# Kernel optimization log

Measured on AMD Instinct MI355X. Metric: run time of the kernel, lower is better.

## Reference

```python
import jax, jax.numpy as jnp
import numpy as np

BN_EPS = 1e-5
STRIDE = 4
K_NEAREST = 16


def _fps(xyz, m):
    """Farthest point sampling. xyz: [n,3] -> indices [m] (seeded at point 0)."""
    n = xyz.shape[0]

    def body(i, state):
        dist, idxs, last = state
        d = jnp.sum((xyz - xyz[last]) ** 2, axis=-1)
        dist = jnp.minimum(dist, d)
        nxt = jnp.argmax(dist).astype(jnp.int32)
        return dist, idxs.at[i].set(nxt), nxt

    init = (jnp.full((n,), 1e10, xyz.dtype), jnp.zeros((m,), jnp.int32), jnp.int32(0))
    _, idxs, _ = jax.lax.fori_loop(1, m, body, init)
    return idxs


def _knn(q, x, k):
    """q: [m,3] queries, x: [n,3] points -> [m,k] nearest-neighbor indices."""
    d = jnp.sum((q[:, None, :] - x[None, :, :]) ** 2, axis=-1)  # [m,n]
    _, idx = jax.lax.top_k(-d, k)
    return idx


def setup_inputs() -> dict:
    key = jax.random.key(0)
    k0, k1, k2 = jax.random.split(key, 3)
    B, N, IN_CH, OUT_CH = 4, 8192, 64, 128
    events = jax.random.uniform(k0, (B, N, 4), dtype=jnp.float32)  # xyz in [0,1) + time
    features = jax.random.normal(k1, (B, N, IN_CH), dtype=jnp.float32)
    W = jax.random.normal(k2, (4 + IN_CH, OUT_CH), dtype=jnp.float32) / np.float32(np.sqrt(4 + IN_CH))
    b = jnp.zeros((OUT_CH,), jnp.float32)
    gamma = jnp.ones((OUT_CH,), jnp.float32)
    beta = jnp.zeros((OUT_CH,), jnp.float32)
    return dict(events=events, features=features, W=W, b=b, gamma=gamma, beta=beta)


def reference(events, features, W, b, gamma, beta):
    B, N, _ = events.shape
    m = N // STRIDE  # down_offsets = offsets // stride with equal-size samples
    xyz = events[..., :3]
    xyz_c = jax.lax.stop_gradient(xyz)  # indices are non-differentiable

    # farthest point sampling per cloud -> [B, m]
    down_idx = jax.vmap(lambda p: _fps(p, m))(xyz_c)
    down_xyz = jnp.take_along_axis(xyz_c, down_idx[..., None], axis=1)  # [B,m,3]
    # k nearest neighbors of each sampled point -> [B, m, K]
    idx = jax.vmap(lambda q, x: _knn(q, x, K_NEAREST))(down_xyz, xyz_c)

    down_events = jnp.take_along_axis(events, down_idx[..., None], axis=1)  # [B,m,4]
    grouped_events = jax.vmap(lambda e, i: e[i])(events, idx)               # [B,m,K,4]
    grouped_events_norm = grouped_events - down_events[:, :, None, :]
    grouped_features = jax.vmap(lambda f, i: f[i])(features, idx)           # [B,m,K,in_ch]
    g = jnp.concatenate([grouped_events_norm, grouped_features], axis=-1)   # [B,m,K,4+in_ch]

    # Linear -> BatchNorm1d (training batch stats over all points & neighbors) -> ReLU
    h = jnp.einsum('bmkc,cd->bmkd', g, W) + b
    mu = jnp.mean(h, axis=(0, 1, 2))
    var = jnp.var(h, axis=(0, 1, 2))
    h = (h - mu) * jax.lax.rsqrt(var + BN_EPS) * gamma + beta
    h = jax.nn.relu(h)

    down_features = jnp.max(h, axis=2)  # max-pool over K neighbors -> [B,m,out_ch]
    return down_events, down_features
```

## Files before the change

### kernel.cpp

```cpp
#include <hip/hip_runtime.h>

#define N_PTS 8192
#define M_PTS 2048
#define K_NN 16
#define IN_CH 64
#define G_CH 68
#define OUT_CH 128
#define KCAP 128

__device__ __forceinline__ float subrn(float a, float b) {
    float r; asm("v_sub_f32 %0, %1, %2" : "=v"(r) : "v"(a), "v"(b)); return r;
}
__device__ __forceinline__ float mulrn(float a, float b) {
    float r; asm("v_mul_f32 %0, %1, %2" : "=v"(r) : "v"(a), "v"(b)); return r;
}
__device__ __forceinline__ float addrn(float a, float b) {
    float r; asm("v_add_f32 %0, %1, %2" : "=v"(r) : "v"(a), "v"(b)); return r;
}
__device__ __forceinline__ float sqdist_rn(float ax, float ay, float az,
                                           float bx, float by, float bz) {
    float dx = subrn(ax, bx);
    float dy = subrn(ay, by);
    float dz = subrn(az, bz);
    return addrn(addrn(mulrn(dx, dx), mulrn(dy, dy)), mulrn(dz, dz));
}

typedef float v2f __attribute__((ext_vector_type(2)));
__device__ __forceinline__ v2f pk_add(v2f a, v2f b) {
    v2f r; asm("v_pk_add_f32 %0, %1, %2" : "=v"(r) : "v"(a), "v"(b)); return r;
}
__device__ __forceinline__ v2f pk_mul(v2f a, v2f b) {
    v2f r; asm("v_pk_mul_f32 %0, %1, %2" : "=v"(r) : "v"(a), "v"(b)); return r;
}

template <int CTRL>
__device__ __forceinline__ float movdpp_f(float x) {
    int r = __builtin_amdgcn_mov_dpp(__float_as_int(x), CTRL, 0xf, 0xf, true);
    return __int_as_float(r);
}
template <int CTRL, int RM>
__device__ __forceinline__ float dppmaxf_m(float x) {
    int r = __builtin_amdgcn_update_dpp(0, __float_as_int(x), CTRL, RM, 0xf, false);
    return fmaxf(x, __int_as_float(r));
}
__device__ __forceinline__ float wave_max64(float x) {
    x = fmaxf(x, movdpp_f<0xB1>(x));
    x = fmaxf(x, movdpp_f<0x4E>(x));
    x = fmaxf(x, movdpp_f<0x141>(x));
    x = fmaxf(x, movdpp_f<0x140>(x));
    x = dppmaxf_m<0x142, 0xa>(x);
    x = dppmaxf_m<0x143, 0xc>(x);
    return x;
}
__device__ __forceinline__ float group8_max(float x) {
    x = fmaxf(x, movdpp_f<0xB1>(x));
    x = fmaxf(x, movdpp_f<0x4E>(x));
    x = fmaxf(x, movdpp_f<0x141>(x));
    return x;
}

__global__ __launch_bounds__(512, 2) void fps_kernel(const float4* __restrict__ events4,
                                                     int* __restrict__ down_idx,
                                                     float4* __restrict__ out_de) {
    extern __shared__ char smem[];
    float*  rv   = (float*)smem;
    int*    wsl  = (int*)(smem + 32);
    int*    ssel = (int*)(smem + 64);
    float4* spt  = (float4*)(smem + 64 + 4 * M_PTS);

    const int b = blockIdx.x;
    const int tid = threadIdx.x;
    const int wave = tid >> 6;
    const int lane = tid & 63;
    const float4* ev = events4 + (size_t)b * N_PTS;

    for (int i = tid; i < N_PTS; i += 512) spt[i] = ev[i];
    if (tid == 0) { ssel[0] = 0; wsl[0] = 0x7fffffff; wsl[1] = 0x7fffffff; }
    __syncthreads();

    v2f px[8], py[8], pz[8];
    float dist[16];
#pragma unroll
    for (int pp = 0; pp < 8; ++pp) {
        float4 f0 = spt[(2 * pp) * 512 + tid];
        float4 f1 = spt[(2 * pp + 1) * 512 + tid];
        px[pp] = (v2f){f0.x, f1.x};
        py[pp] = (v2f){f0.y, f1.y};
        pz[pp] = (v2f){f0.z, f1.z};
        dist[2 * pp] = 1e10f; dist[2 * pp + 1] = 1e10f;
    }

    int last = 0;
    for (int i = 1; i < M_PTS; ++i) {
        float4 L = spt[last];
        const float nlx = -L.x, nly = -L.y, nlz = -L.z;
        const v2f nx2 = (v2f){nlx, nlx};
        const v2f ny2 = (v2f){nly, nly};
        const v2f nz2 = (v2f){nlz, nlz};
#pragma unroll
        for (int pp = 0; pp < 8; ++pp) {
            v2f dx = pk_add(px[pp], nx2);
            v2f dy = pk_add(py[pp], ny2);
            v2f dz = pk_add(pz[pp], nz2);
            v2f s  = pk_add(pk_add(pk_mul(dx, dx), pk_mul(dy, dy)), pk_mul(dz, dz));
            dist[2 * pp]     = fminf(dist[2 * pp],     s.x);
            dist[2 * pp + 1] = fminf(dist[2 * pp + 1], s.y);
        }
        float t0[8];
#pragma unroll
        for (int j = 0; j < 8; ++j) t0[j] = fmaxf(dist[2 * j], dist[2 * j + 1]);
#pragma unroll
        for (int j = 0; j < 4; ++j) t0[j] = fmaxf(t0[2 * j], t0[2 * j + 1]);
        float bd = fmaxf(fmaxf(t0[0], t0[1]), fmaxf(t0[2], t0[3]));

        float wm = wave_max64(bd);
        if (lane == 63) rv[wave] = wm;
        __syncthreads();
        float bm = group8_max(rv[lane & 7]);

        if (bd == bm) {
            int jm = 0;
#pragma unroll
            for (int j = 15; j >= 0; --j) if (dist[j] == bd) jm = j;
            atomicMin(&wsl[i & 1], jm * 512 + tid);
        }
        __syncthreads();
        last = wsl[i & 1];
        if (tid == 0) { ssel[i] = last; wsl[(i + 1) & 1] = 0x7fffffff; }
    }
    __syncthreads();

    for (int i = tid; i < M_PTS; i += 512) {
        int s = ssel[i];
        down_idx[b * M_PTS + i] = s;
        out_de[(size_t)b * M_PTS + i] = spt[s];
    }
}

__global__ __launch_bounds__(256, 1) void knn_kernel(const float4* __restrict__ events4,
                                                     const int* __restrict__ down_idx,
                                                     int* __restrict__ knn_idx) {
    extern __shared__ char smem[];
    float2* sxy  = (float2*)smem;
    float*  sz   = (float*)(smem + N_PTS * 8);
    float*  cd   = sz + N_PTS;
    int*    ci   = (int*)(cd + 32 * KCAP);
    int*    scnt = (int*)(ci + 32 * KCAP);

    const int b    = blockIdx.x >> 6;
    const int qg   = blockIdx.x & 63;
    const int tid  = threadIdx.x;
    const int ql   = tid >> 3;
    const int part = tid & 7;

    const float4* ev = events4 + (size_t)b * N_PTS;
    for (int i = tid; i < N_PTS; i += 256) {
        float4 e = ev[i];
        sxy[i] = (float2){e.x, e.y}; sz[i] = e.z;
    }
    if (tid < 32) scnt[tid] = 0;
    __syncthreads();

    const int q  = qg * 32 + ql;
    const int qi = down_idx[b * M_PTS + q];
    const float2 qxy = sxy[qi];
    const float qx = qxy.x, qy = qxy.y, qz = sz[qi];

    const float4* sxy4 = (const float4*)sxy;
    const float2* sz2  = (const float2*)sz;

    float m1 = 1e30f, m2 = 1e30f;
    for (int i = 0; i < N_PTS / 16; ++i) {
        const int ph = i * 8 + part;
        float4 xy = sxy4[ph];
        float2 zz = sz2[ph];
        float d0 = sqdist_rn(xy.x, xy.y, zz.x, qx, qy, qz);
        float d1 = sqdist_rn(xy.z, xy.w, zz.y, qx, qy, qz);
        float lo0 = fminf(m1, d0);
        m2 = fminf(m2, fmaxf(m1, d0));
        m1 = lo0;
        float lo1 = fminf(m1, d1);
        m2 = fminf(m2, fmaxf(m1, d1));
        m1 = lo1;
    }
    const float T = group8_max(m2);

    for (int i = 0; i < N_PTS / 16; ++i) {
        const int ph = i * 8 + part;
        float4 xy = sxy4[ph];
        float2 zz = sz2[ph];
        float d0 = sqdist_rn(xy.x, xy.y, zz.x, qx, qy, qz);
        float d1 = sqdist_rn(xy.z, xy.w, zz.y, qx, qy, qz);
        if (d0 <= T) {
            int pos = atomicAdd(&scnt[ql], 1);
            if (pos < KCAP) { cd[ql * KCAP + pos] = d0; ci[ql * KCAP + pos] = 2 * ph; }
        }
        if (d1 <= T) {
            int pos = atomicAdd(&scnt[ql], 1);
            if (pos < KCAP) { cd[ql * KCAP + pos] = d1; ci[ql * KCAP + pos] = 2 * ph + 1; }
        }
    }
    __syncthreads();

    if (part == 0) {
        float nd[16]; int ni[16];
#pragma unroll
        for (int j = 0; j < 16; ++j) { nd[j] = 1e30f; ni[j] = 0x7fffffff; }
        float wmax = 1e30f; int widx = 0x7fffffff; int wslot = 0;
        const int n = scnt[ql];
        const int lim = (n <= KCAP) ? n : 0;
        for (int t = 0; t < lim; ++t) {
            float d = cd[ql * KCAP + t];
            int   p = ci[ql * KCAP + t];
            if (d < wmax || (d == wmax && p < widx)) {
#pragma unroll
                for (int j = 0; j < 16; ++j) if (j == wslot) { nd[j] = d; ni[j] = p; }
                float m_ = -1.0f; int mix_ = -1; int ms_ = 0;
#pragma unroll
                for (int j = 0; j < 16; ++j)
                    if (nd[j] > m_ || (nd[j] == m_ && ni[j] > mix_)) { m_ = nd[j]; mix_ = ni[j]; ms_ = j; }
                wmax = m_; widx = mix_; wslot = ms_;
            }
        }
        if (n > KCAP) {
            for (int p = 0; p < N_PTS; ++p) {
                float2 pxy = sxy[p];
                float d = sqdist_rn(pxy.x, pxy.y, sz[p], qx, qy, qz);
                if (d < wmax || (d == wmax && p < widx)) {
#pragma unroll
                    for (int j = 0; j < 16; ++j) if (j == wslot) { nd[j] = d; ni[j] = p; }
                    float m_ = -1.0f; int mix_ = -1; int ms_ = 0;
#pragma unroll
                    for (int j = 0; j < 16; ++j)
                        if (nd[j] > m_ || (nd[j] == m_ && ni[j] > mix_)) { m_ = nd[j]; mix_ = ni[j]; ms_ = j; }
                    wmax = m_; widx = mix_; wslot = ms_;
                }
            }
        }
        int* out = knn_idx + ((size_t)(b * M_PTS + q)) * K_NN;
#pragma unroll
        for (int j = 0; j < 16; ++j) out[j] = ni[j];
    }
}

__global__ __launch_bounds__(256, 2) void gmm_kernel(const float4* __restrict__ events4,
                                                     const float4* __restrict__ feat4,
                                                     const float* __restrict__ W,
                                                     const float* __restrict__ bias,
                                                     const int* __restrict__ knn_idx,
                                                     const float4* __restrict__ de4,
                                                     float* __restrict__ hmax_g,
                                                     float* __restrict__ hmin_g,
                                                     float* __restrict__ gsum,
                                                     float* __restrict__ gsq) {
    __shared__ __align__(16) float4 sg4[2 * 16 * 17];
    __shared__ float scomb[2 * OUT_CH];

    const int b   = blockIdx.x >> 7;
    const int qg  = blockIdx.x & 127;
    const int tid = threadIdx.x;
    const int d   = tid & 127;
    const int qs  = tid >> 7;

    float w[G_CH];
#pragma unroll
    for (int c = 0; c < G_CH; ++c) w[c] = W[c * OUT_CH + d];
    const float breg = bias[d];

    float ssum = 0.f, ssq = 0.f;

    for (int r = 0; r < 8; ++r) {
        const int base = b * M_PTS + qg * 16 + 2 * r;
        for (int j4 = tid; j4 < 2 * 16 * 17; j4 += 256) {
            int qq = j4 / 272;
            int rem = j4 - qq * 272;
            int k = rem / 17;
            int c4 = rem - k * 17;
            int nb = knn_idx[(base + qq) * K_NN + k];
            float4 v;
            if (c4 == 0) {
                float4 e = events4[(size_t)b * N_PTS + nb];
                float4 d0 = de4[base + qq];
                v = (float4){e.x - d0.x, e.y - d0.y, e.z - d0.z, e.w - d0.w};
            } else {
                v = feat4[((size_t)(b * N_PTS + nb)) * 16 + (c4 - 1)];
            }
            sg4[j4] = v;
        }
        __syncthreads();

        float hmax = -1e30f, hmin = 1e30f;
#pragma unroll
        for (int k = 0; k < 16; ++k) {
            float acc = breg;
#pragma unroll
            for (int c4 = 0; c4 < 17; ++c4) {
                float4 g = sg4[qs * 272 + k * 17 + c4];
                acc = fmaf(g.x, w[4 * c4 + 0], acc);
                acc = fmaf(g.y, w[4 * c4 + 1], acc);
                acc = fmaf(g.z, w[4 * c4 + 2], acc);
                acc = fmaf(g.w, w[4 * c4 + 3], acc);
            }
            hmax = fmaxf(hmax, acc);
            hmin = fminf(hmin, acc);
            ssum += acc;
            ssq = fmaf(acc, acc, ssq);
        }
        const size_t o = (size_t)(base + qs) * OUT_CH + d;
        hmax_g[o] = hmax;
        hmin_g[o] = hmin;
        __syncthreads();
    }

    if (qs == 1) { scomb[d] = ssum; scomb[OUT_CH + d] = ssq; }
    __syncthreads();
    if (qs == 0) {
        atomicAdd(&gsum[d], ssum + scomb[d]);
        atomicAdd(&gsq[d],  ssq  + scomb[OUT_CH + d]);
    }
}

__global__ __launch_bounds__(256) void fin_kernel(const float* __restrict__ hmax_g,
                                                  const float* __restrict__ hmin_g,
                                                  const float* __restrict__ gsum,
                                                  const float* __restrict__ gsq,
                                                  const float* __restrict__ gamma,
                                                  const float* __restrict__ beta,
                                                  float* __restrict__ out) {
    const size_t e = (size_t)blockIdx.x * 256 + threadIdx.x;
    const int d = (int)(e & 127);
    const float inv_cnt = 1.0f / 131072.0f;
    float mu  = gsum[d] * inv_cnt;
    float var = gsq[d] * inv_cnt - mu * mu;
    float a   = gamma[d] * rsqrtf(var + 1e-5f);
    float sh  = fmaf(-mu, a, beta[d]);
    float hv  = (a >= 0.f) ? hmax_g[e] : hmin_g[e];
    float r   = fmaf(a, hv, sh);
    out[32768 + e] = r > 0.f ? r : 0.f;
}

extern "C" void kernel_launch(void* const* d_in, const int* in_sizes, int n_in,
                              void* d_out, int out_size, void* d_ws, size_t ws_size,
                              hipStream_t stream) {
    const float* events   = (const float*)d_in[0];
    const float* features = (const float*)d_in[1];
    const float* W        = (const float*)d_in[2];
    const float* bias     = (const float*)d_in[3];
    const float* gamma    = (const float*)d_in[4];
    const float* beta     = (const float*)d_in[5];
    float* out = (float*)d_out;
    char* ws = (char*)d_ws;

    int*   down_idx = (int*)ws;
    int*   knn_idx  = (int*)(ws + 32768);
    float* gsum     = (float*)(ws + 32768 + 524288);
    float* gsq      = gsum + OUT_CH;
    float* hmaxg    = (float*)(ws + 558080);
    float* hming    = hmaxg + (size_t)4 * M_PTS * OUT_CH;

    (void)hipMemsetAsync(gsum, 0, 2 * OUT_CH * sizeof(float), stream);

    const size_t fps_lds = 64 + 4 * M_PTS + (size_t)N_PTS * sizeof(float4);
    fps_kernel<<<4, 512, fps_lds, stream>>>((const float4*)events, down_idx, (float4*)out);

    const size_t knn_lds = (size_t)N_PTS * 8 + (size_t)N_PTS * 4
                         + (size_t)32 * KCAP * 8 + 128;
    knn_kernel<<<256, 256, knn_lds, stream>>>((const float4*)events, down_idx, knn_idx);

    gmm_kernel<<<512, 256, 0, stream>>>((const float4*)events, (const float4*)features,
                                        W, bias, knn_idx, (const float4*)out,
                                        hmaxg, hming, gsum, gsq);

    fin_kernel<<<4096, 256, 0, stream>>>(hmaxg, hming, gsum, gsq, gamma, beta, out);
}
```

Before: 2.376 ms.

## Fuse FPS, KNN and grouped MLP into one persistent kernel with progress flags

Merges the three kernels into one launch. Four blocks run farthest point sampling and publish progress through global atomic counters. The remaining 252 blocks wait on those counters and then run KNN and the grouped linear/stat accumulation for chunks of 16 queries. This overlaps the serial FPS with the KNN and matmul work, which previously ran only after FPS finished, and drops the knn_idx round trip through global memory. KNN now uses 32 lanes per query with a single-min threshold and a larger candidate cap. The spin-waits depend on the FPS blocks being co-resident, and the looser threshold may send more queries to the slow fallback path.

```diff
diff --git a/kernel.cpp b/kernel.cpp
--- a/kernel.cpp
+++ b/kernel.cpp
@@ -6,7 +6,10 @@
 #define IN_CH 64
 #define G_CH 68
 #define OUT_CH 128
-#define KCAP 128
+#define KC 192
+#define NWK 63
+#define CHQ 16
+#define NCHUNK (M_PTS / CHQ)
 
 __device__ __forceinline__ float subrn(float a, float b) {
     float r; asm("v_sub_f32 %0, %1, %2" : "=v"(r) : "v"(a), "v"(b)); return r;
@@ -58,177 +61,201 @@
     x = fmaxf(x, movdpp_f<0x141>(x));
     return x;
 }
-
-__global__ __launch_bounds__(512, 2) void fps_kernel(const float4* __restrict__ events4,
-                                                     int* __restrict__ down_idx,
-                                                     float4* __restrict__ out_de) {
+__device__ __forceinline__ float group32_max(float x) {
+    x = fmaxf(x, movdpp_f<0xB1>(x));
+    x = fmaxf(x, movdpp_f<0x4E>(x));
+    x = fmaxf(x, movdpp_f<0x141>(x));
+    x = fmaxf(x, movdpp_f<0x140>(x));
+    x = fmaxf(x, __shfl_xor(x, 16));
+    return x;
+}
+
+__global__ __launch_bounds__(512, 2) void fused_kernel(
+        const float4* __restrict__ events4,
+        const float4* __restrict__ feat4,
+        const float*  __restrict__ W,
+        const float*  __restrict__ bias,
+        int*   __restrict__ down_idx,
+        int*   __restrict__ prog,
+        float4* __restrict__ out_de,
+        float* __restrict__ hmax_g,
+        float* __restrict__ hmin_g,
+        float* __restrict__ gsum,
+        float* __restrict__ gsq) {
     extern __shared__ char smem[];
-    float*  rv   = (float*)smem;
-    int*    wsl  = (int*)(smem + 32);
-    int*    ssel = (int*)(smem + 64);
-    float4* spt  = (float4*)(smem + 64 + 4 * M_PTS);
-
-    const int b = blockIdx.x;
     const int tid = threadIdx.x;
-    const int wave = tid >> 6;
-    const int lane = tid & 63;
+
+    if (blockIdx.x < 4) {
+        float*  rv   = (float*)smem;
+        int*    wsl  = (int*)(smem + 32);
+        int*    ssel = (int*)(smem + 64);
+        float4* spt  = (float4*)(smem + 64 + 4 * M_PTS);
+
+        const int b = blockIdx.x;
+        const int wave = tid >> 6;
+        const int lane = tid & 63;
+        const float4* ev = events4 + (size_t)b * N_PTS;
+
+        for (int i = tid; i < N_PTS; i += 512) spt[i] = ev[i];
+        if (tid == 0) {
+            ssel[0] = 0; wsl[0] = 0x7fffffff; wsl[1] = 0x7fffffff;
+            down_idx[b * M_PTS] = 0;
+        }
+        __syncthreads();
+
+        v2f px[8], py[8], pz[8];
+        float dist[16];
+#pragma unroll
+        for (int pp = 0; pp < 8; ++pp) {
+            float4 f0 = spt[(2 * pp) * 512 + tid];
+            float4 f1 = spt[(2 * pp + 1) * 512 + tid];
+            px[pp] = (v2f){f0.x, f1.x};
+            py[pp] = (v2f){f0.y, f1.y};
+            pz[pp] = (v2f){f0.z, f1.z};
+            dist[2 * pp] = 1e10f; dist[2 * pp + 1] = 1e10f;
+        }
+
+        int last = 0;
+        for (int i = 1; i < M_PTS; ++i) {
+            float4 L = spt[last];
+            const float nlx = -L.x, nly = -L.y, nlz = -L.z;
+            const v2f nx2 = (v2f){nlx, nlx};
+            const v2f ny2 = (v2f){nly, nly};
+            const v2f nz2 = (v2f){nlz, nlz};
+#pragma unroll
+            for (int pp = 0; pp < 8; ++pp) {
+                v2f dx = pk_add(px[pp], nx2);
+                v2f dy = pk_add(py[pp], ny2);
+                v2f dz = pk_add(pz[pp], nz2);
+                v2f s  = pk_add(pk_add(pk_mul(dx, dx), pk_mul(dy, dy)), pk_mul(dz, dz));
+                dist[2 * pp]     = fminf(dist[2 * pp],     s.x);
+                dist[2 * pp + 1] = fminf(dist[2 * pp + 1], s.y);
+            }
+            float t0[8];
+#pragma unroll
+            for (int j = 0; j < 8; ++j) t0[j] = fmaxf(dist[2 * j], dist[2 * j + 1]);
+#pragma unroll
+            for (int j = 0; j < 4; ++j) t0[j] = fmaxf(t0[2 * j], t0[2 * j + 1]);
+            float bd = fmaxf(fmaxf(t0[0], t0[1]), fmaxf(t0[2], t0[3]));
+
+            float wm = wave_max64(bd);
+            if (lane == 63) rv[wave] = wm;
+            __syncthreads();
+            float bm = group8_max(rv[lane & 7]);
+
+            if (bd == bm) {
+                int jm = 0;
+#pragma unroll
+                for (int j = 15; j >= 0; --j) if (dist[j] == bd) jm = j;
+                atomicMin(&wsl[i & 1], jm * 512 + tid);
+            }
+            __syncthreads();
+            last = wsl[i & 1];
+            if (tid == 0) {
+                ssel[i] = last;
+                down_idx[b * M_PTS + i] = last;
+                wsl[(i + 1) & 1] = 0x7fffffff;
+                if ((i & 31) == 31)
+                    __hip_atomic_store(prog + b, i + 1, __ATOMIC_RELEASE,
+                                       __HIP_MEMORY_SCOPE_AGENT);
+            }
+        }
+        __syncthreads();
+
+        for (int i = tid; i < M_PTS; i += 512) {
+            out_de[(size_t)b * M_PTS + i] = spt[ssel[i]];
+        }
+        return;
+    }
+
+    float2* sxy  = (float2*)smem;
+    float*  szl  = (float*)(smem + 65536);
+    float*  cd   = (float*)(smem + 98304);
+    int*    ci   = (int*)(smem + 98304 + 16 * KC * 4);
+    int*    scnt = (int*)(smem + 98304 + 32 * KC * 4);
+    int*    sqi  = (int*)(smem + 98304 + 32 * KC * 4 + 64);
+    int*    sk   = (int*)(smem + 98304 + 32 * KC * 4 + 128);
+    float4* sg4  = (float4*)(smem + 98304 + 32 * KC * 4 + 1152);
+
+    const int wk = blockIdx.x - 4;
+    const int b  = wk / NWK;
+    const int w  = wk - b * NWK;
+    const int ql   = tid >> 5;
+    const int part = tid & 31;
+    const int d  = tid & 127;
+    const int qs = tid >> 7;
+
     const float4* ev = events4 + (size_t)b * N_PTS;
-
-    for (int i = tid; i < N_PTS; i += 512) spt[i] = ev[i];
-    if (tid == 0) { ssel[0] = 0; wsl[0] = 0x7fffffff; wsl[1] = 0x7fffffff; }
-    __syncthreads();
-
-    v2f px[8], py[8], pz[8];
-    float dist[16];
-#pragma unroll
-    for (int pp = 0; pp < 8; ++pp) {
-        float4 f0 = spt[(2 * pp) * 512 + tid];
-        float4 f1 = spt[(2 * pp + 1) * 512 + tid];
-        px[pp] = (v2f){f0.x, f1.x};
-        py[pp] = (v2f){f0.y, f1.y};
-        pz[pp] = (v2f){f0.z, f1.z};
-        dist[2 * pp] = 1e10f; dist[2 * pp + 1] = 1e10f;
+    for (int i = tid; i < N_PTS; i += 512) {
+        float4 e = ev[i];
+        sxy[i] = (float2){e.x, e.y}; szl[i] = e.z;
     }
 
-    int last = 0;
-    for (int i = 1; i < M_PTS; ++i) {
-        float4 L = spt[last];
-        const float nlx = -L.x, nly = -L.y, nlz = -L.z;
-        const v2f nx2 = (v2f){nlx, nlx};
-        const v2f ny2 = (v2f){nly, nly};
-        const v2f nz2 = (v2f){nlz, nlz};
-#pragma unroll
-        for (int pp = 0; pp < 8; ++pp) {
-            v2f dx = pk_add(px[pp], nx2);
-            v2f dy = pk_add(py[pp], ny2);
-            v2f dz = pk_add(pz[pp], nz2);
-            v2f s  = pk_add(pk_add(pk_mul(dx, dx), pk_mul(dy, dy)), pk_mul(dz, dz));
-            dist[2 * pp]     = fminf(dist[2 * pp],     s.x);
-            dist[2 * pp + 1] = fminf(dist[2 * pp + 1], s.y);
-        }
-        float t0[8];
-#pragma unroll
-        for (int j = 0; j < 8; ++j) t0[j] = fmaxf(dist[2 * j], dist[2 * j + 1]);
-#pragma unroll
-        for (int j = 0; j < 4; ++j) t0[j] = fmaxf(t0[2 * j], t0[2 * j + 1]);
-        float bd = fmaxf(fmaxf(t0[0], t0[1]), fmaxf(t0[2], t0[3]));
-
-        float wm = wave_max64(bd);
-        if (lane == 63) rv[wave] = wm;
-        __syncthreads();
-        float bm = group8_max(rv[lane & 7]);
-
-        if (bd == bm) {
-            int jm = 0;
-#pragma unroll
-            for (int j = 15; j >= 0; --j) if (dist[j] == bd) jm = j;
-            atomicMin(&wsl[i & 1], jm * 512 + tid);
-        }
-        __syncthreads();
-        last = wsl[i & 1];
-        if (tid == 0) { ssel[i] = last; wsl[(i + 1) & 1] = 0x7fffffff; }
-    }
-    __syncthreads();
-
-    for (int i = tid; i < M_PTS; i += 512) {
-        int s = ssel[i];
-        down_idx[b * M_PTS + i] = s;
-        out_de[(size_t)b * M_PTS + i] = spt[s];
-    }
-}
-
-__global__ __launch_bounds__(256, 1) void knn_kernel(const float4* __restrict__ events4,
-                                                     const int* __restrict__ down_idx,
-                                                     int* __restrict__ knn_idx) {
-    extern __shared__ char smem[];
-    float2* sxy  = (float2*)smem;
-    float*  sz   = (float*)(smem + N_PTS * 8);
-    float*  cd   = sz + N_PTS;
-    int*    ci   = (int*)(cd + 32 * KCAP);
-    int*    scnt = (int*)(ci + 32 * KCAP);
-
-    const int b    = blockIdx.x >> 6;
-    const int qg   = blockIdx.x & 63;
-    const int tid  = threadIdx.x;
-    const int ql   = tid >> 3;
-    const int part = tid & 7;
-
-    const float4* ev = events4 + (size_t)b * N_PTS;
-    for (int i = tid; i < N_PTS; i += 256) {
-        float4 e = ev[i];
-        sxy[i] = (float2){e.x, e.y}; sz[i] = e.z;
-    }
-    if (tid < 32) scnt[tid] = 0;
-    __syncthreads();
-
-    const int q  = qg * 32 + ql;
-    const int qi = down_idx[b * M_PTS + q];
-    const float2 qxy = sxy[qi];
-    const float qx = qxy.x, qy = qxy.y, qz = sz[qi];
+    float wreg[G_CH];
+#pragma unroll
+    for (int c = 0; c < G_CH; ++c) wreg[c] = W[c * OUT_CH + d];
+    const float breg = bias[d];
+    float ssum = 0.f, ssq = 0.f;
 
     const float4* sxy4 = (const float4*)sxy;
-    const float2* sz2  = (const float2*)sz;
-
-    float m1 = 1e30f, m2 = 1e30f;
-    for (int i = 0; i < N_PTS / 16; ++i) {
-        const int ph = i * 8 + part;
-        float4 xy = sxy4[ph];
-        float2 zz = sz2[ph];
-        float d0 = sqdist_rn(xy.x, xy.y, zz.x, qx, qy, qz);
-        float d1 = sqdist_rn(xy.z, xy.w, zz.y, qx, qy, qz);
-        float lo0 = fminf(m1, d0);
-        m2 = fminf(m2, fmaxf(m1, d0));
-        m1 = lo0;
-        float lo1 = fminf(m1, d1);
-        m2 = fminf(m2, fmaxf(m1, d1));
-        m1 = lo1;
-    }
-    const float T = group8_max(m2);
-
-    for (int i = 0; i < N_PTS / 16; ++i) {
-        const int ph = i * 8 + part;
-        float4 xy = sxy4[ph];
-        float2 zz = sz2[ph];
-        float d0 = sqdist_rn(xy.x, xy.y, zz.x, qx, qy, qz);
-        float d1 = sqdist_rn(xy.z, xy.w, zz.y, qx, qy, qz);
-        if (d0 <= T) {
-            int pos = atomicAdd(&scnt[ql], 1);
-            if (pos < KCAP) { cd[ql * KCAP + pos] = d0; ci[ql * KCAP + pos] = 2 * ph; }
-        }
-        if (d1 <= T) {
-            int pos = atomicAdd(&scnt[ql], 1);
-            if (pos < KCAP) { cd[ql * KCAP + pos] = d1; ci[ql * KCAP + pos] = 2 * ph + 1; }
-        }
-    }
-    __syncthreads();
-
-    if (part == 0) {
-        float nd[16]; int ni[16];
-#pragma unroll
-        for (int j = 0; j < 16; ++j) { nd[j] = 1e30f; ni[j] = 0x7fffffff; }
-        float wmax = 1e30f; int widx = 0x7fffffff; int wslot = 0;
-        const int n = scnt[ql];
-        const int lim = (n <= KCAP) ? n : 0;
-        for (int t = 0; t < lim; ++t) {
-            float d = cd[ql * KCAP + t];
-            int   p = ci[ql * KCAP + t];
-            if (d < wmax || (d == wmax && p < widx)) {
-#pragma unroll
-                for (int j = 0; j < 16; ++j) if (j == wslot) { nd[j] = d; ni[j] = p; }
-                float m_ = -1.0f; int mix_ = -1; int ms_ = 0;
-#pragma unroll
-                for (int j = 0; j < 16; ++j)
-                    if (nd[j] > m_ || (nd[j] == m_ && ni[j] > mix_)) { m_ = nd[j]; mix_ = ni[j]; ms_ = j; }
-                wmax = m_; widx = mix_; wslot = ms_;
-            }
-        }
-        if (n > KCAP) {
-            for (int p = 0; p < N_PTS; ++p) {
-                float2 pxy = sxy[p];
-                float d = sqdist_rn(pxy.x, pxy.y, sz[p], qx, qy, qz);
-                if (d < wmax || (d == wmax && p < widx)) {
-#pragma unroll
-                    for (int j = 0; j < 16; ++j) if (j == wslot) { nd[j] = d; ni[j] = p; }
+    const float2* sz2  = (const float2*)szl;
+
+    for (int s = 0; s < 3; ++s) {
+        const int c = w + s * NWK;
+        if (c >= NCHUNK) break;
+        const int need = (c + 1) * CHQ;
+        while (__hip_atomic_load(prog + b, __ATOMIC_ACQUIRE,
+                                 __HIP_MEMORY_SCOPE_AGENT) < need)
+            __builtin_amdgcn_s_sleep(16);
+        if (tid < CHQ) scnt[tid] = 0;
+        __syncthreads();
+
+        const int q  = c * CHQ + ql;
+        const int qi = down_idx[b * M_PTS + q];
+        const float2 qxy = sxy[qi];
+        const float qx = qxy.x, qy = qxy.y, qz = szl[qi];
+
+        float m1 = 1e30f;
+        for (int i = 0; i < 128; ++i) {
+            const int ph = i * 32 + part;
+            float4 xy = sxy4[ph];
+            float2 zz = sz2[ph];
+            float d0 = sqdist_rn(xy.x, xy.y, zz.x, qx, qy, qz);
+            float d1 = sqdist_rn(xy.z, xy.w, zz.y, qx, qy, qz);
+            m1 = fminf(m1, fminf(d0, d1));
+        }
+        const float T = group32_max(m1);
+
+        for (int i = 0; i < 128; ++i) {
+            const int ph = i * 32 + part;
+            float4 xy = sxy4[ph];
+            float2 zz = sz2[ph];
+            float d0 = sqdist_rn(xy.x, xy.y, zz.x, qx, qy, qz);
+            float d1 = sqdist_rn(xy.z, xy.w, zz.y, qx, qy, qz);
+            if (d0 <= T) {
+                int pos = atomicAdd(&scnt[ql], 1);
+                if (pos < KC) { cd[ql * KC + pos] = d0; ci[ql * KC + pos] = 2 * ph; }
+            }
+            if (d1 <= T) {
+                int pos = atomicAdd(&scnt[ql], 1);
+                if (pos < KC) { cd[ql * KC + pos] = d1; ci[ql * KC + pos] = 2 * ph + 1; }
+            }
+        }
+        __syncthreads();
+
+        if (part == 0) {
+            float nd[16]; int ni[16];
+#pragma unroll
+            for (int j = 0; j < 16; ++j) { nd[j] = 1e30f; ni[j] = 0x7fffffff; }
+            float wmax = 1e30f; int widx = 0x7fffffff; int wslot = 0;
+            const int n = scnt[ql];
+            const int lim = (n <= KC) ? n : 0;
+            for (int t = 0; t < lim; ++t) {
+                float dv = cd[ql * KC + t];
+                int   p  = ci[ql * KC + t];
+                if (dv < wmax || (dv == wmax && p < widx)) {
+#pragma unroll
+                    for (int j = 0; j < 16; ++j) if (j == wslot) { nd[j] = dv; ni[j] = p; }
                     float m_ = -1.0f; int mix_ = -1; int ms_ = 0;
 #pragma unroll
                     for (int j = 0; j < 16; ++j)
@@ -236,88 +263,80 @@
                     wmax = m_; widx = mix_; wslot = ms_;
                 }
             }
-        }
-        int* out = knn_idx + ((size_t)(b * M_PTS + q)) * K_NN;
-#pragma unroll
-        for (int j = 0; j < 16; ++j) out[j] = ni[j];
+            if (n > KC) {
+                for (int p = 0; p < N_PTS; ++p) {
+                    float2 pxy = sxy[p];
+                    float dv = sqdist_rn(pxy.x, pxy.y, szl[p], qx, qy, qz);
+                    if (dv < wmax || (dv == wmax && p < widx)) {
+#pragma unroll
+                        for (int j = 0; j < 16; ++j) if (j == wslot) { nd[j] = dv; ni[j] = p; }
+                        float m_ = -1.0f; int mix_ = -1; int ms_ = 0;
+#pragma unroll
+                        for (int j = 0; j < 16; ++j)
+                            if (nd[j] > m_ || (nd[j] == m_ && ni[j] > mix_)) { m_ = nd[j]; mix_ = ni[j]; ms_ = j; }
+                        wmax = m_; widx = mix_; wslot = ms_;
+                    }
+                }
+            }
+            sqi[ql] = qi;
+#pragma unroll
+            for (int j = 0; j < 16; ++j) sk[ql * 16 + j] = ni[j];
+        }
+        __syncthreads();
+
+        for (int r4 = 0; r4 < 4; ++r4) {
+            for (int j4 = tid; j4 < 4 * 16 * 17; j4 += 512) {
+                int qq  = j4 / 272;
+                int rem = j4 - qq * 272;
+                int k   = rem / 17;
+                int c4  = rem - k * 17;
+                int qlo = r4 * 4 + qq;
+                int nb  = sk[qlo * 16 + k];
+                float4 v;
+                if (c4 == 0) {
+                    float4 e  = events4[(size_t)b * N_PTS + nb];
+                    float4 d0 = events4[(size_t)b * N_PTS + sqi[qlo]];
+                    v = (float4){e.x - d0.x, e.y - d0.y, e.z - d0.z, e.w - d0.w};
+                } else {
+                    v = feat4[((size_t)(b * N_PTS + nb)) * 16 + (c4 - 1)];
+                }
+                sg4[j4] = v;
+            }
+            __syncthreads();
+
+            const int qlo = r4 * 4 + qs;
+            float hmax = -1e30f, hmin = 1e30f;
+#pragma unroll
+            for (int k = 0; k < 16; ++k) {
+                float acc = breg;
+#pragma unroll
+                for (int c4 = 0; c4 < 17; ++c4) {
+                    float4 g = sg4[qs * 272 + k * 17 + c4];
+                    acc = fmaf(g.x, wreg[4 * c4 + 0], acc);
+                    acc = fmaf(g.y, wreg[4 * c4 + 1], acc);
+                    acc = fmaf(g.z, wreg[4 * c4 + 2], acc);
+                    acc = fmaf(g.w, wreg[4 * c4 + 3], acc);
+                }
+                hmax = fmaxf(hmax, acc);
+                hmin = fminf(hmin, acc);
+                ssum += acc;
+                ssq = fmaf(acc, acc, ssq);
+            }
+            const size_t o = ((size_t)(b * M_PTS + c * CHQ + qlo)) * OUT_CH + d;
+            hmax_g[o] = hmax;
+            hmin_g[o] = hmin;
+            __syncthreads();
+        }
     }
-}
-
-__global__ __launch_bounds__(256, 2) void gmm_kernel(const float4* __restrict__ events4,
-                                                     const float4* __restrict__ feat4,
-                                                     const float* __restrict__ W,
-                                                     const float* __restrict__ bias,
-                                                     const int* __restrict__ knn_idx,
-                                                     const float4* __restrict__ de4,
-                                                     float* __restrict__ hmax_g,
-                                                     float* __restrict__ hmin_g,
-                                                     float* __restrict__ gsum,
-                                                     float* __restrict__ gsq) {
-    __shared__ __align__(16) float4 sg4[2 * 16 * 17];
-    __shared__ float scomb[2 * OUT_CH];
-
-    const int b   = blockIdx.x >> 7;
-    const int qg  = blockIdx.x & 127;
-    const int tid = threadIdx.x;
-    const int d   = tid & 127;
-    const int qs  = tid >> 7;
-
-    float w[G_CH];
-#pragma unroll
-    for (int c = 0; c < G_CH; ++c) w[c] = W[c * OUT_CH + d];
-    const float breg = bias[d];
-
-    float ssum = 0.f, ssq = 0.f;
-
-    for (int r = 0; r < 8; ++r) {
-        const int base = b * M_PTS + qg * 16 + 2 * r;
-        for (int j4 = tid; j4 < 2 * 16 * 17; j4 += 256) {
-            int qq = j4 / 272;
-            int rem = j4 - qq * 272;
-            int k = rem / 17;
-            int c4 = rem - k * 17;
-            int nb = knn_idx[(base + qq) * K_NN + k];
-            float4 v;
-            if (c4 == 0) {
-                float4 e = events4[(size_t)b * N_PTS + nb];
-                float4 d0 = de4[base + qq];
-                v = (float4){e.x - d0.x, e.y - d0.y, e.z - d0.z, e.w - d0.w};
-            } else {
-                v = feat4[((size_t)(b * N_PTS + nb)) * 16 + (c4 - 1)];
-            }
-            sg4[j4] = v;
-        }
-        __syncthreads();
-
-        float hmax = -1e30f, hmin = 1e30f;
-#pragma unroll
-        for (int k = 0; k < 16; ++k) {
-            float acc = breg;
-#pragma unroll
-            for (int c4 = 0; c4 < 17; ++c4) {
-                float4 g = sg4[qs * 272 + k * 17 + c4];
-                acc = fmaf(g.x, w[4 * c4 + 0], acc);
-                acc = fmaf(g.y, w[4 * c4 + 1], acc);
-                acc = fmaf(g.z, w[4 * c4 + 2], acc);
-                acc = fmaf(g.w, w[4 * c4 + 3], acc);
-            }
-            hmax = fmaxf(hmax, acc);
-            hmin = fminf(hmin, acc);
-            ssum += acc;
-            ssq = fmaf(acc, acc, ssq);
-        }
-        const size_t o = (size_t)(base + qs) * OUT_CH + d;
-        hmax_g[o] = hmax;
-        hmin_g[o] = hmin;
-        __syncthreads();
-    }
-
-    if (qs == 1) { scomb[d] = ssum; scomb[OUT_CH + d] = ssq; }
+
+    float* red = cd;
+    red[tid] = ssum;
     __syncthreads();
-    if (qs == 0) {
-        atomicAdd(&gsum[d], ssum + scomb[d]);
-        atomicAdd(&gsq[d],  ssq  + scomb[OUT_CH + d]);
-    }
+    if (tid < 128) atomicAdd(&gsum[tid], red[tid] + red[tid + 128] + red[tid + 256] + red[tid + 384]);
+    __syncthreads();
+    red[tid] = ssq;
+    __syncthreads();
+    if (tid < 128) atomicAdd(&gsq[tid],  red[tid] + red[tid + 128] + red[tid + 256] + red[tid + 384]);
 }
 
 __global__ __launch_bounds__(256) void fin_kernel(const float* __restrict__ hmax_g,
@@ -352,24 +371,19 @@
     char* ws = (char*)d_ws;
 
     int*   down_idx = (int*)ws;
-    int*   knn_idx  = (int*)(ws + 32768);
-    float* gsum     = (float*)(ws + 32768 + 524288);
-    float* gsq      = gsum + OUT_CH;
-    float* hmaxg    = (float*)(ws + 558080);
+    float* gsum     = (float*)(ws + 32768);
+    float* gsq      = (float*)(ws + 33280);
+    int*   prog     = (int*)(ws + 33792);
+    float* hmaxg    = (float*)(ws + 40960);
     float* hming    = hmaxg + (size_t)4 * M_PTS * OUT_CH;
 
-    (void)hipMemsetAsync(gsum, 0, 2 * OUT_CH * sizeof(float), stream);
-
-    const size_t fps_lds = 64 + 4 * M_PTS + (size_t)N_PTS * sizeof(float4);
-    fps_kernel<<<4, 512, fps_lds, stream>>>((const float4*)events, down_idx, (float4*)out);
-
-    const size_t knn_lds = (size_t)N_PTS * 8 + (size_t)N_PTS * 4
-                         + (size_t)32 * KCAP * 8 + 128;
-    knn_kernel<<<256, 256, knn_lds, stream>>>((const float4*)events, down_idx, knn_idx);
-
-    gmm_kernel<<<512, 256, 0, stream>>>((const float4*)events, (const float4*)features,
-                                        W, bias, knn_idx, (const float4*)out,
-                                        hmaxg, hming, gsum, gsq);
+    (void)hipMemsetAsync(gsum, 0, 1024, stream);
+    (void)hipMemsetAsync(prog, 0, 256, stream);
+
+    const size_t lds = 141440;
+    fused_kernel<<<256, 512, lds, stream>>>((const float4*)events, (const float4*)features,
+                                            W, bias, down_idx, prog, (float4*)out,
+                                            hmaxg, hming, gsum, gsq);
 
     fin_kernel<<<4096, 256, 0, stream>>>(hmaxg, hming, gsum, gsq, gamma, beta, out);
 }
```

After: 3.472 ms. 46.1% more time.
